# Performance work log

Hardware: AMD Instinct MI355X
Metric: run time of the kernel (lower is better)

The kernel has to match this reference:

```python
import jax, jax.numpy as jnp
import numpy as np
from jax import lax

KS = 5            # patch kernel size
STRIDE = 4        # patch stride / scale ratio
SHIFTS = (2, 2)   # roll shifts before patch extraction
SOFTMAX_SCALE = 10.0
MID_CH = 64
BAND_HS = 8


def same_pad(x, k, s):
    """TensorFlow-style SAME padding for kernel k, stride s (NCHW)."""
    H, W = x.shape[-2], x.shape[-1]
    oh, ow = -(-H // s), -(-W // s)
    ph = max(0, (oh - 1) * s + k - H)
    pw = max(0, (ow - 1) * s + k - W)
    return jnp.pad(x, ((0, 0), (0, 0), (ph // 2, ph - ph // 2), (pw // 2, pw - pw // 2)))


def extract_patches(x, k, s, shifts):
    """torch.nn.Unfold equivalent with SAME padding and roll -> [N, L, C, k, k]."""
    x = same_pad(x, k, s)
    x = jnp.roll(x, shifts[0], axis=2)
    x = jnp.roll(x, shifts[1], axis=3)
    p = lax.conv_general_dilated_patches(
        x, (k, k), (s, s), 'VALID', dimension_numbers=('NCHW', 'OIHW', 'NCHW'))
    N, _, Hn, Wn = p.shape
    C = x.shape[1]
    # channel ordering is (C, kh, kw) channel-slowest, matching torch unfold
    return p.reshape(N, C, k, k, Hn * Wn).transpose(0, 4, 1, 2, 3)


def conv3(x, w, b):
    """3x3 conv, padding=1, bias + LeakyReLU(0.01) (BasicBlock)."""
    y = lax.conv_general_dilated(x, w, (1, 1), [(1, 1), (1, 1)],
                                 dimension_numbers=('NCHW', 'OIHW', 'NCHW'))
    return jax.nn.leaky_relu(y + b[None, :, None, None], 0.01)


def setup_inputs() -> dict:
    key = jax.random.key(0)
    ks = jax.random.split(key, 11)
    f32 = jnp.float32
    return {
        'ms':   jax.random.normal(ks[0], (2, BAND_HS, 96, 96), f32),
        'pan':  jax.random.normal(ks[1], (2, 1, 384, 384), f32),
        'pan2': jax.random.normal(ks[2], (2, 1, 96, 96), f32),
        'wq': jax.random.normal(ks[3], (MID_CH, 1, 3, 3), f32) * 0.1,
        'bq': jax.random.normal(ks[4], (MID_CH,), f32) * 0.02,
        'wk': jax.random.normal(ks[5], (MID_CH, 1, 3, 3), f32) * 0.1,
        'bk': jax.random.normal(ks[6], (MID_CH,), f32) * 0.02,
        'wv': jax.random.normal(ks[7], (BAND_HS, BAND_HS, 3, 3), f32) * 0.1,
        'bv': jax.random.normal(ks[8], (BAND_HS,), f32) * 0.02,
        'wr': jax.random.normal(ks[9], (BAND_HS, BAND_HS, 3, 3), f32) * 0.1,
        'br': jax.random.normal(ks[10], (BAND_HS,), f32) * 0.02,
    }


def reference(ms, pan, pan2, wq, bq, wk, bk, wv, bv, wr, br):
    k_fea = conv3(pan2, wk, bk)                       # [N, mid, h, w]
    q_fea = conv3(pan, wq, bq)                        # [N, mid, H, W]
    v_fea = conv3(ms, wv, bv)                         # [N, band, h, w]

    k_patch = extract_patches(k_fea, KS, STRIDE, SHIFTS)  # [N, L, mid, ks, ks]
    v_patch = extract_patches(v_fea, KS, STRIDE, SHIFTS)  # [N, L, band, ks, ks]

    def attend(q, kp, vp):
        # q: [mid, H, W]; kp: [L, mid, ks, ks]; vp: [L, band, ks, ks]
        norms = jnp.sqrt(jnp.sum(kp * kp, axis=(1, 2, 3)))      # per-patch L2 norms
        k0 = kp / jnp.max(norms)                                # global-max normalization
        q0 = same_pad(q[None], KS, STRIDE)                      # [1, mid, Hp, Wp]
        scores = lax.conv_general_dilated(
            q0, k0, (STRIDE, STRIDE), 'VALID',
            dimension_numbers=('NCHW', 'OIHW', 'NCHW'))          # [1, L, H', W']
        attn = jax.nn.softmax(scores * SOFTMAX_SCALE, axis=1)
        # conv_transpose2d(attn, vp, stride) == dilated conv with flipped, transposed kernel
        wT = jnp.flip(vp, (2, 3)).transpose(1, 0, 2, 3)          # [band, L, ks, ks]
        out = lax.conv_general_dilated(
            attn, wT, (1, 1), [(KS - 1, KS - 1)] * 2,
            lhs_dilation=(STRIDE, STRIDE),
            dimension_numbers=('NCHW', 'OIHW', 'NCHW'))          # [1, band, Ho, Wo]
        return out[0] / 6.0

    res = jax.vmap(attend)(q_fea, k_patch, v_patch)   # [N, band, Ho, Wo]
    return conv3(res, wr, br)
```

## Files before the change

### kernel.cpp

```cpp
#include <hip/hip_runtime.h>
#include <math.h>


typedef _Float16 f16;
typedef _Float16 f16x8 __attribute__((ext_vector_type(8)));
typedef float f32x4 __attribute__((ext_vector_type(4)));

namespace csa {
constexpr int NB   = 2;
constexpr int MID  = 64;
constexpr int BAND = 8;
constexpr int HK   = 96;
constexpr int HQ   = 384;
constexpr int HQP  = 385;
constexpr int LN   = 24;
constexpr int L    = 576;
constexpr int LP   = 640;
constexpr int PS   = 96 * 96;
constexpr int KDIM = MID * 25;
constexpr int VDIM = BAND * 25;
constexpr int MV   = 256;
constexpr int HO   = 385;
constexpr size_t QCLN = (size_t)HQP * HQP * MID;

constexpr size_t align256(size_t x) { return (x + 255) & ~(size_t)255; }
constexpr size_t OFF_QCL  = 0;
constexpr size_t OFF_KCL  = align256(OFF_QCL + (size_t)NB*QCLN*2);
constexpr size_t OFF_VFEA = align256(OFF_KCL + (size_t)NB*HK*HK*MID*2);
constexpr size_t OFF_N2   = align256(OFF_VFEA + (size_t)NB*BAND*HK*HK*4);
constexpr size_t OFF_SC   = align256(OFF_N2   + (size_t)NB*L*4);
constexpr size_t OFF_KM   = align256(OFF_SC   + 256);
constexpr size_t OFF_VT   = align256(OFF_KM   + (size_t)NB*LP*KDIM*2);
constexpr size_t OFF_ST   = align256(OFF_VT   + (size_t)NB*MV*L*2);
constexpr size_t OFF_AT   = align256(OFF_ST   + (size_t)NB*PS*LP*4);
constexpr size_t OFF_D    = align256(OFF_AT   + (size_t)NB*PS*L*2);
constexpr size_t OFF_RES  = align256(OFF_D    + (size_t)NB*MV*PS*4);
}
using namespace csa;

__global__ __launch_bounds__(256) void csa_conv_cl(
    const float* __restrict__ in, const float* __restrict__ w,
    const float* __restrict__ b, f16* __restrict__ out, int H, int Hout) {
  int id = blockIdx.x * 256 + threadIdx.x;
  int total = NB * Hout * Hout;
  if (id >= total) return;
  int x = id % Hout;
  int t = id / Hout;
  int y = t % Hout;
  int n = t / Hout;
  f16* op = out + (size_t)id * MID;
  if (y >= H || x >= H) {
    f16x8 z = {0, 0, 0, 0, 0, 0, 0, 0};
#pragma unroll
    for (int c8 = 0; c8 < 8; ++c8) *(f16x8*)(op + c8 * 8) = z;
    return;
  }
  const float* ip = in + (size_t)n * H * H;
  float p[9];
#pragma unroll
  for (int dy = 0; dy < 3; ++dy)
#pragma unroll
    for (int dx = 0; dx < 3; ++dx) {
      int yy = y + dy - 1, xx = x + dx - 1;
      p[dy * 3 + dx] = (yy >= 0 && yy < H && xx >= 0 && xx < H)
                           ? ip[(size_t)yy * H + xx] : 0.f;
    }
#pragma unroll
  for (int c8 = 0; c8 < 8; ++c8) {
    f16x8 o;
#pragma unroll
    for (int e = 0; e < 8; ++e) {
      int co = c8 * 8 + e;
      float acc = b[co];
#pragma unroll
      for (int k = 0; k < 9; ++k) acc = fmaf(p[k], w[co * 9 + k], acc);
      o[e] = (f16)(acc > 0.f ? acc : 0.01f * acc);
    }
    *(f16x8*)(op + c8 * 8) = o;
  }
}

__global__ __launch_bounds__(256) void csa_conv3_8x8(
    const float* __restrict__ in, const float* __restrict__ w,
    const float* __restrict__ b, float* __restrict__ out, int H, int W) {
  int id = blockIdx.x * 256 + threadIdx.x;
  int total = NB * H * W;
  if (id >= total) return;
  int x = id % W;
  int t = id / W;
  int y = t % H;
  int n = t / H;
  const float* ip = in + (size_t)n * BAND * H * W;
  float p[BAND][9];
#pragma unroll
  for (int ci = 0; ci < BAND; ++ci)
#pragma unroll
    for (int dy = 0; dy < 3; ++dy)
#pragma unroll
      for (int dx = 0; dx < 3; ++dx) {
        int yy = y + dy - 1, xx = x + dx - 1;
        p[ci][dy * 3 + dx] = (yy >= 0 && yy < H && xx >= 0 && xx < W)
                                 ? ip[((size_t)ci * H + yy) * W + xx] : 0.f;
      }
  float* op = out + ((size_t)n * BAND * H + y) * W + x;
  for (int co = 0; co < BAND; ++co) {
    float acc = b[co];
#pragma unroll
    for (int ci = 0; ci < BAND; ++ci)
#pragma unroll
      for (int k = 0; k < 9; ++k)
        acc = fmaf(p[ci][k], w[(co * BAND + ci) * 9 + k], acc);
    acc = acc > 0.f ? acc : 0.01f * acc;
    op[(size_t)co * H * W] = acc;
  }
}

__global__ __launch_bounds__(256) void csa_build_patches(
    const f16* __restrict__ kcl, const float* __restrict__ v_fea,
    f16* __restrict__ Kmat, f16* __restrict__ Vt, float* __restrict__ n2) {
  int blk = blockIdx.x;
  int n = blk / LP;
  int l = blk % LP;
  int tid = threadIdx.x;
  f16* krow = Kmat + ((size_t)n * LP + l) * KDIM;
  if (l >= L) {
    f16x8 z = {0, 0, 0, 0, 0, 0, 0, 0};
    for (int ch = tid; ch < 200; ch += 256) *(f16x8*)(krow + ch * 8) = z;
    return;
  }
  int i = l / LN, j = l % LN;
  const f16* kn = kcl + (size_t)n * HK * HK * MID;
  float ss = 0.f;
  for (int ch = tid; ch < 200; ch += 256) {
    int khkw = ch >> 3;
    int c0 = (ch & 7) * 8;
    int kh = khkw / 5, kw = khkw % 5;
    int r = (4 * i + kh + 95) % 97;
    int cc = (4 * j + kw + 95) % 97;
    f16x8 v = {0, 0, 0, 0, 0, 0, 0, 0};
    if (r < HK && cc < HK)
      v = *(const f16x8*)(kn + ((size_t)r * HK + cc) * MID + c0);
#pragma unroll
    for (int e = 0; e < 8; ++e) {
      float f = (float)v[e];
      ss += f * f;
    }
    *(f16x8*)(krow + ch * 8) = v;
  }
  for (int m = tid; m < MV; m += 256) {
    float v = 0.f;
    if (m < VDIM) {
      int kw = m % 5;
      int t = m / 5;
      int kh = t % 5;
      int c = t / 5;
      int r = (4 * i + kh + 95) % 97;
      int cc = (4 * j + kw + 95) % 97;
      v = (r < HK && cc < HK)
              ? v_fea[(((size_t)n * BAND + c) * HK + r) * HK + cc] : 0.f;
    }
    Vt[((size_t)n * MV + m) * L + l] = (f16)v;
  }
  __shared__ float red[256];
  red[tid] = ss;
  __syncthreads();
  for (int s = 128; s > 0; s >>= 1) {
    if (tid < s) red[tid] += red[tid + s];
    __syncthreads();
  }
  if (tid == 0) n2[n * L + l] = red[0];
}

__global__ __launch_bounds__(256) void csa_max_scale(
    const float* __restrict__ n2, float* __restrict__ scale) {
  int n = blockIdx.x;
  int tid = threadIdx.x;
  float m = 0.f;
  for (int l = tid; l < L; l += 256) m = fmaxf(m, n2[n * L + l]);
  __shared__ float red[256];
  red[tid] = m;
  __syncthreads();
  for (int s = 128; s > 0; s >>= 1) {
    if (tid < s) red[tid] = fmaxf(red[tid], red[tid + s]);
    __syncthreads();
  }
  if (tid == 0) scale[n] = 10.f / sqrtf(red[0]);
}

__device__ __forceinline__ void gl_lds16(const f16* g, f16* s) {
  __builtin_amdgcn_global_load_lds(
      (const __attribute__((address_space(1))) void*)g,
      (__attribute__((address_space(3))) void*)s, 16, 0, 0);
}

__global__ __launch_bounds__(256) void csa_gemm1(
    const f16* __restrict__ qcl, const f16* __restrict__ Km,
    float* __restrict__ C) {
  __shared__ __attribute__((aligned(16))) f16 As[4096];
  __shared__ __attribute__((aligned(16))) f16 Bs[4096];
  const int tid = threadIdx.x;
  const int w = tid >> 6;
  const int l = tid & 63;
  const int q = l >> 4;
  const int r = l & 15;
  const int nb = blockIdx.z;
  qcl += (size_t)nb * QCLN;
  Km += (size_t)nb * LP * KDIM;
  C += (size_t)nb * (size_t)PS * LP;
  const int bm = blockIdx.y * 128;
  const int bn = blockIdx.x * 128;
  const int wm = (w >> 1) * 64;
  const int wn = (w & 1) * 64;

  f32x4 acc[4][4];
#pragma unroll
  for (int i = 0; i < 4; ++i)
#pragma unroll
    for (int j = 0; j < 4; ++j) {
      f32x4 z = {0.f, 0.f, 0.f, 0.f};
      acc[i][j] = z;
    }

  const int p0 = bm + w * 16 + r;
  const int y0 = p0 / 96, x0 = p0 % 96;
  const int p1 = p0 + 64;
  const int y1 = p1 / 96, x1 = p1 % 96;
  const f16* a0 = qcl + ((size_t)(4 * y0) * HQP + 4 * x0) * MID + q * 8;
  const f16* a1 = qcl + ((size_t)(4 * y1) * HQP + 4 * x1) * MID + q * 8;
  const f16* gb0 = Km + (size_t)(bn + w * 16 + r) * KDIM + q * 8;
  const f16* gb1 = gb0 + (size_t)64 * KDIM;
  f16* lA0 = As + w * 512;
  f16* lA1 = As + 2048 + w * 512;
  f16* lB0 = Bs + w * 512;
  f16* lB1 = Bs + 2048 + w * 512;
  const int am = (w >> 1) * 4;
  const int bnn = (w & 1) * 4;

  int t = 0;
  for (int kh = 0; kh < 5; ++kh) {
    for (int kw = 0; kw < 5; ++kw) {
      const size_t offA = ((size_t)kh * HQP + kw) * MID;
#pragma unroll
      for (int half = 0; half < 2; ++half, ++t) {
        const size_t oA = offA + half * 32;
        const size_t oB = (size_t)t * 32;
        gl_lds16(a0 + oA, lA0);
        gl_lds16(a1 + oA, lA1);
        gl_lds16(gb0 + oB, lB0);
        gl_lds16(gb1 + oB, lB1);
        __syncthreads();
        f16x8 af[4], bf[4];
#pragma unroll
        for (int u = 0; u < 4; ++u) {
          af[u] = *(const f16x8*)&As[(am + u) * 512 + q * 128 + r * 8];
          bf[u] = *(const f16x8*)&Bs[(bnn + u) * 512 + q * 128 + r * 8];
        }
#pragma unroll
        for (int i = 0; i < 4; ++i)
#pragma unroll
          for (int j = 0; j < 4; ++j)
            acc[i][j] = __builtin_amdgcn_mfma_f32_16x16x32_f16(af[i], bf[j],
                                                               acc[i][j], 0, 0, 0);
        __syncthreads();
      }
    }
  }
  const int cn = bn + wn + r;
#pragma unroll
  for (int i = 0; i < 4; ++i) {
    int rm = bm + wm + i * 16 + q * 4;
#pragma unroll
    for (int j = 0; j < 4; ++j)
#pragma unroll
      for (int rr = 0; rr < 4; ++rr)
        C[(size_t)(rm + rr) * LP + cn + j * 16] = acc[i][j][rr];
  }
}

__global__ __launch_bounds__(256) void csa_gemm_f16(
    const f16* __restrict__ A, const f16* __restrict__ Bt,
    float* __restrict__ C, int M, int N, int K,
    size_t strideA, size_t strideB, size_t strideC) {
  __shared__ __attribute__((aligned(16))) f16 As[4096];
  __shared__ __attribute__((aligned(16))) f16 Bs[4096];
  const int tid = threadIdx.x;
  const int w = tid >> 6;
  const int l = tid & 63;
  const int q = l >> 4;
  const int r = l & 15;
  const int nb = blockIdx.z;
  A += (size_t)nb * strideA;
  Bt += (size_t)nb * strideB;
  C += (size_t)nb * strideC;
  const int bm = blockIdx.y * 128;
  const int bn = blockIdx.x * 128;
  const int wm = (w >> 1) * 64;
  const int wn = (w & 1) * 64;

  f32x4 acc[4][4];
#pragma unroll
  for (int i = 0; i < 4; ++i)
#pragma unroll
    for (int j = 0; j < 4; ++j) {
      f32x4 z = {0.f, 0.f, 0.f, 0.f};
      acc[i][j] = z;
    }

  const f16* ga0 = A + (size_t)(bm + w * 16 + r) * K + q * 8;
  const f16* ga1 = ga0 + (size_t)64 * K;
  const f16* gb0 = Bt + (size_t)(bn + w * 16 + r) * K + q * 8;
  const f16* gb1 = gb0 + (size_t)64 * K;
  f16* lA0 = As + w * 512;
  f16* lA1 = As + 2048 + w * 512;
  f16* lB0 = Bs + w * 512;
  f16* lB1 = Bs + 2048 + w * 512;
  const int am = (w >> 1) * 4;
  const int bnn = (w & 1) * 4;

  for (int k0 = 0; k0 < K; k0 += 32) {
    gl_lds16(ga0 + k0, lA0);
    gl_lds16(ga1 + k0, lA1);
    gl_lds16(gb0 + k0, lB0);
    gl_lds16(gb1 + k0, lB1);
    __syncthreads();
    f16x8 af[4], bf[4];
#pragma unroll
    for (int u = 0; u < 4; ++u) {
      af[u] = *(const f16x8*)&As[(am + u) * 512 + q * 128 + r * 8];
      bf[u] = *(const f16x8*)&Bs[(bnn + u) * 512 + q * 128 + r * 8];
    }
#pragma unroll
    for (int i = 0; i < 4; ++i)
#pragma unroll
      for (int j = 0; j < 4; ++j)
        acc[i][j] =
            __builtin_amdgcn_mfma_f32_16x16x32_f16(af[i], bf[j], acc[i][j], 0, 0, 0);
    __syncthreads();
  }

  const int cn = bn + wn + r;
#pragma unroll
  for (int i = 0; i < 4; ++i) {
    int rm = bm + wm + i * 16 + q * 4;
#pragma unroll
    for (int j = 0; j < 4; ++j)
#pragma unroll
      for (int rr = 0; rr < 4; ++rr)
        C[(size_t)(rm + rr) * N + cn + j * 16] = acc[i][j][rr];
  }
}

__global__ __launch_bounds__(256) void csa_softmax(
    const float* __restrict__ scoresT, const float* __restrict__ scale,
    f16* __restrict__ attnT) {
  const int wv = threadIdx.x >> 6;
  const int lane = threadIdx.x & 63;
  const int p = blockIdx.x * 4 + wv;
  const int n = blockIdx.y;
  const float sc = scale[n];
  const float* row = scoresT + ((size_t)n * PS + p) * LP;
  float v[9];
  float m = -1e30f;
#pragma unroll
  for (int j = 0; j < 9; ++j) {
    v[j] = row[lane + j * 64] * sc;
    m = fmaxf(m, v[j]);
  }
#pragma unroll
  for (int off = 32; off > 0; off >>= 1) m = fmaxf(m, __shfl_xor(m, off));
  float e[9], s = 0.f;
#pragma unroll
  for (int j = 0; j < 9; ++j) {
    e[j] = __expf(v[j] - m);
    s += e[j];
  }
#pragma unroll
  for (int off = 32; off > 0; off >>= 1) s += __shfl_xor(s, off);
  const float inv = 1.f / s;
  f16* orow = attnT + ((size_t)n * PS + p) * L;
#pragma unroll
  for (int j = 0; j < 9; ++j) orow[lane + j * 64] = (f16)(e[j] * inv);
}

__global__ __launch_bounds__(256) void csa_gather(
    const float* __restrict__ D, float* __restrict__ res) {
  int id = blockIdx.x * 256 + threadIdx.x;
  if (id >= NB * BAND * HO * HO) return;
  int ox = id % HO;
  int t = id / HO;
  int oy = t % HO;
  t = t / HO;
  int co = t % BAND;
  int n = t / BAND;
  const float* Dn = D + (size_t)n * MV * PS;
  float s = 0.f;
  int kh0 = oy & 3;
  int kw0 = ox & 3;
  for (int kh = kh0; kh < 5; kh += 4) {
    int y = (oy - kh) >> 2;
    if (y < 0 || y >= 96) continue;
    for (int kw = kw0; kw < 5; kw += 4) {
      int x = (ox - kw) >> 2;
      if (x < 0 || x >= 96) continue;
      s += Dn[(size_t)(co * 25 + kh * 5 + kw) * PS + y * 96 + x];
    }
  }
  res[id] = s * (1.f / 6.f);
}

extern "C" void kernel_launch(void* const* d_in, const int* in_sizes, int n_in,
                              void* d_out, int out_size, void* d_ws,
                              size_t ws_size, hipStream_t stream) {
  const float* ms   = (const float*)d_in[0];
  const float* pan  = (const float*)d_in[1];
  const float* pan2 = (const float*)d_in[2];
  const float* wq = (const float*)d_in[3];
  const float* bq = (const float*)d_in[4];
  const float* wk = (const float*)d_in[5];
  const float* bk = (const float*)d_in[6];
  const float* wv = (const float*)d_in[7];
  const float* bv = (const float*)d_in[8];
  const float* wr = (const float*)d_in[9];
  const float* br = (const float*)d_in[10];
  float* out = (float*)d_out;

  char* ws = (char*)d_ws;
  f16*   qcl   = (f16*)(ws + OFF_QCL);
  f16*   kcl   = (f16*)(ws + OFF_KCL);
  float* v_fea = (float*)(ws + OFF_VFEA);
  float* n2    = (float*)(ws + OFF_N2);
  float* scale = (float*)(ws + OFF_SC);
  f16*   Kmat  = (f16*)(ws + OFF_KM);
  f16*   Vt    = (f16*)(ws + OFF_VT);
  float* scoT  = (float*)(ws + OFF_ST);
  f16*   attnT = (f16*)(ws + OFF_AT);
  float* Dm    = (float*)(ws + OFF_D);
  float* res   = (float*)(ws + OFF_RES);

  dim3 b256(256);
  csa_conv_cl<<<dim3((NB * HQP * HQP + 255) / 256), b256, 0, stream>>>(
      pan, wq, bq, qcl, HQ, HQP);
  csa_conv_cl<<<dim3((NB * HK * HK + 255) / 256), b256, 0, stream>>>(
      pan2, wk, bk, kcl, HK, HK);
  csa_conv3_8x8<<<dim3((NB * HK * HK + 255) / 256), b256, 0, stream>>>(
      ms, wv, bv, v_fea, HK, HK);
  csa_build_patches<<<dim3(NB * LP), b256, 0, stream>>>(kcl, v_fea, Kmat, Vt,
                                                        n2);
  csa_max_scale<<<dim3(NB), b256, 0, stream>>>(n2, scale);

  csa_gemm1<<<dim3(LP / 128, PS / 128, NB), b256, 0, stream>>>(qcl, Kmat,
                                                               scoT);

  csa_softmax<<<dim3(PS / 4, NB), b256, 0, stream>>>(scoT, scale, attnT);

  csa_gemm_f16<<<dim3(PS / 128, MV / 128, NB), b256, 0, stream>>>(
      Vt, attnT, Dm, MV, PS, L,
      (size_t)MV * L, (size_t)PS * L, (size_t)MV * PS);

  csa_gather<<<dim3((NB * BAND * HO * HO + 255) / 256), b256, 0, stream>>>(
      Dm, res);
  csa_conv3_8x8<<<dim3((NB * HO * HO + 255) / 256), b256, 0, stream>>>(
      res, wr, br, out, HO, HO);
}
```

Before: 302.6 us.

## Store Q features in stride-4 phase-split layout for contiguous GEMM A loads

The query conv output is now written in a polyphase layout [n][x-phase][y][x/4][ch], so the stride-4 patch rows read by the scores GEMM sit next to each other in memory. Before, each lane read 128-byte channel vectors spaced 4 pixels apart. The wider, coalesced A-tile loads are meant to cut wasted memory traffic in gemm1. In exchange the conv writes a slightly larger buffer with an extra padded column, the address math becomes more complex, and the zero padding at the edges has to be handled correctly.

```diff
diff --git a/kernel.cpp b/kernel.cpp
--- a/kernel.cpp
+++ b/kernel.cpp
@@ -13,6 +13,7 @@
 constexpr int HK   = 96;
 constexpr int HQ   = 384;
 constexpr int HQP  = 385;
+constexpr int XI   = 97;
 constexpr int LN   = 24;
 constexpr int L    = 576;
 constexpr int LP   = 640;
@@ -21,11 +22,11 @@
 constexpr int VDIM = BAND * 25;
 constexpr int MV   = 256;
 constexpr int HO   = 385;
-constexpr size_t QCLN = (size_t)HQP * HQP * MID;
+constexpr size_t QPSN = (size_t)4 * HQP * XI * MID;
 
 constexpr size_t align256(size_t x) { return (x + 255) & ~(size_t)255; }
-constexpr size_t OFF_QCL  = 0;
-constexpr size_t OFF_KCL  = align256(OFF_QCL + (size_t)NB*QCLN*2);
+constexpr size_t OFF_QPS  = 0;
+constexpr size_t OFF_KCL  = align256(OFF_QPS + (size_t)NB*QPSN*2);
 constexpr size_t OFF_VFEA = align256(OFF_KCL + (size_t)NB*HK*HK*MID*2);
 constexpr size_t OFF_N2   = align256(OFF_VFEA + (size_t)NB*BAND*HK*HK*4);
 constexpr size_t OFF_SC   = align256(OFF_N2   + (size_t)NB*L*4);
@@ -38,23 +39,62 @@
 }
 using namespace csa;
 
+__global__ __launch_bounds__(256) void csa_convq_ps(
+    const float* __restrict__ in, const float* __restrict__ w,
+    const float* __restrict__ b, f16* __restrict__ out) {
+  int id = blockIdx.x * 256 + threadIdx.x;
+  int total = NB * 4 * HQP * XI;
+  if (id >= total) return;
+  int xi = id % XI;
+  int t = id / XI;
+  int yp = t % HQP;
+  t /= HQP;
+  int f = t % 4;
+  int n = t / 4;
+  int xp = 4 * xi + f;
+  f16* op = out + (size_t)id * MID;
+  if (yp >= HQ || xp >= HQ) {
+    f16x8 z = {0, 0, 0, 0, 0, 0, 0, 0};
+#pragma unroll
+    for (int c8 = 0; c8 < 8; ++c8) *(f16x8*)(op + c8 * 8) = z;
+    return;
+  }
+  const float* ip = in + (size_t)n * HQ * HQ;
+  float p[9];
+#pragma unroll
+  for (int dy = 0; dy < 3; ++dy)
+#pragma unroll
+    for (int dx = 0; dx < 3; ++dx) {
+      int yy = yp + dy - 1, xx = xp + dx - 1;
+      p[dy * 3 + dx] = (yy >= 0 && yy < HQ && xx >= 0 && xx < HQ)
+                           ? ip[(size_t)yy * HQ + xx] : 0.f;
+    }
+#pragma unroll
+  for (int c8 = 0; c8 < 8; ++c8) {
+    f16x8 o;
+#pragma unroll
+    for (int e = 0; e < 8; ++e) {
+      int co = c8 * 8 + e;
+      float acc = b[co];
+#pragma unroll
+      for (int k = 0; k < 9; ++k) acc = fmaf(p[k], w[co * 9 + k], acc);
+      o[e] = (f16)(acc > 0.f ? acc : 0.01f * acc);
+    }
+    *(f16x8*)(op + c8 * 8) = o;
+  }
+}
+
 __global__ __launch_bounds__(256) void csa_conv_cl(
     const float* __restrict__ in, const float* __restrict__ w,
-    const float* __restrict__ b, f16* __restrict__ out, int H, int Hout) {
+    const float* __restrict__ b, f16* __restrict__ out, int H) {
   int id = blockIdx.x * 256 + threadIdx.x;
-  int total = NB * Hout * Hout;
+  int total = NB * H * H;
   if (id >= total) return;
-  int x = id % Hout;
-  int t = id / Hout;
-  int y = t % Hout;
-  int n = t / Hout;
+  int x = id % H;
+  int t = id / H;
+  int y = t % H;
+  int n = t / H;
   f16* op = out + (size_t)id * MID;
-  if (y >= H || x >= H) {
-    f16x8 z = {0, 0, 0, 0, 0, 0, 0, 0};
-#pragma unroll
-    for (int c8 = 0; c8 < 8; ++c8) *(f16x8*)(op + c8 * 8) = z;
-    return;
-  }
   const float* ip = in + (size_t)n * H * H;
   float p[9];
 #pragma unroll
@@ -142,8 +182,8 @@
       v = *(const f16x8*)(kn + ((size_t)r * HK + cc) * MID + c0);
 #pragma unroll
     for (int e = 0; e < 8; ++e) {
-      float f = (float)v[e];
-      ss += f * f;
+      float fv = (float)v[e];
+      ss += fv * fv;
     }
     *(f16x8*)(krow + ch * 8) = v;
   }
@@ -194,7 +234,7 @@
 }
 
 __global__ __launch_bounds__(256) void csa_gemm1(
-    const f16* __restrict__ qcl, const f16* __restrict__ Km,
+    const f16* __restrict__ qps, const f16* __restrict__ Km,
     float* __restrict__ C) {
   __shared__ __attribute__((aligned(16))) f16 As[4096];
   __shared__ __attribute__((aligned(16))) f16 Bs[4096];
@@ -204,7 +244,7 @@
   const int q = l >> 4;
   const int r = l & 15;
   const int nb = blockIdx.z;
-  qcl += (size_t)nb * QCLN;
+  qps += (size_t)nb * QPSN;
   Km += (size_t)nb * LP * KDIM;
   C += (size_t)nb * (size_t)PS * LP;
   const int bm = blockIdx.y * 128;
@@ -221,12 +261,12 @@
       acc[i][j] = z;
     }
 
-  const int p0 = bm + w * 16 + r;
-  const int y0 = p0 / 96, x0 = p0 % 96;
-  const int p1 = p0 + 64;
-  const int y1 = p1 / 96, x1 = p1 % 96;
-  const f16* a0 = qcl + ((size_t)(4 * y0) * HQP + 4 * x0) * MID + q * 8;
-  const f16* a1 = qcl + ((size_t)(4 * y1) * HQP + 4 * x1) * MID + q * 8;
+  const int pg0 = bm + w * 16;
+  const int y0 = pg0 / 96, x0 = pg0 % 96;
+  const int pg1 = pg0 + 64;
+  const int y1 = pg1 / 96, x1 = pg1 % 96;
+  const int la = r * MID + q * 8;
+
   const f16* gb0 = Km + (size_t)(bn + w * 16 + r) * KDIM + q * 8;
   const f16* gb1 = gb0 + (size_t)64 * KDIM;
   f16* lA0 = As + w * 512;
@@ -239,13 +279,16 @@
   int t = 0;
   for (int kh = 0; kh < 5; ++kh) {
     for (int kw = 0; kw < 5; ++kw) {
-      const size_t offA = ((size_t)kh * HQP + kw) * MID;
+      const size_t u0 =
+          (((size_t)(kw & 3) * HQP + (4 * y0 + kh)) * XI + x0 + (kw >> 2)) * MID;
+      const size_t u1 =
+          (((size_t)(kw & 3) * HQP + (4 * y1 + kh)) * XI + x1 + (kw >> 2)) * MID;
 #pragma unroll
       for (int half = 0; half < 2; ++half, ++t) {
-        const size_t oA = offA + half * 32;
+        const size_t oA = (size_t)half * 32 + la;
         const size_t oB = (size_t)t * 32;
-        gl_lds16(a0 + oA, lA0);
-        gl_lds16(a1 + oA, lA1);
+        gl_lds16(qps + u0 + oA, lA0);
+        gl_lds16(qps + u1 + oA, lA1);
         gl_lds16(gb0 + oB, lB0);
         gl_lds16(gb1 + oB, lB1);
         __syncthreads();
@@ -425,7 +468,7 @@
   float* out = (float*)d_out;
 
   char* ws = (char*)d_ws;
-  f16*   qcl   = (f16*)(ws + OFF_QCL);
+  f16*   qps   = (f16*)(ws + OFF_QPS);
   f16*   kcl   = (f16*)(ws + OFF_KCL);
   float* v_fea = (float*)(ws + OFF_VFEA);
   float* n2    = (float*)(ws + OFF_N2);
@@ -438,17 +481,17 @@
   float* res   = (float*)(ws + OFF_RES);
 
   dim3 b256(256);
-  csa_conv_cl<<<dim3((NB * HQP * HQP + 255) / 256), b256, 0, stream>>>(
-      pan, wq, bq, qcl, HQ, HQP);
+  csa_convq_ps<<<dim3((NB * 4 * HQP * XI + 255) / 256), b256, 0, stream>>>(
+      pan, wq, bq, qps);
   csa_conv_cl<<<dim3((NB * HK * HK + 255) / 256), b256, 0, stream>>>(
-      pan2, wk, bk, kcl, HK, HK);
+      pan2, wk, bk, kcl, HK);
   csa_conv3_8x8<<<dim3((NB * HK * HK + 255) / 256), b256, 0, stream>>>(
       ms, wv, bv, v_fea, HK, HK);
   csa_build_patches<<<dim3(NB * LP), b256, 0, stream>>>(kcl, v_fea, Kmat, Vt,
                                                         n2);
   csa_max_scale<<<dim3(NB), b256, 0, stream>>>(n2, scale);
 
-  csa_gemm1<<<dim3(LP / 128, PS / 128, NB), b256, 0, stream>>>(qcl, Kmat,
+  csa_gemm1<<<dim3(LP / 128, PS / 128, NB), b256, 0, stream>>>(qps, Kmat,
                                                                scoT);
 
   csa_softmax<<<dim3(PS / 4, NB), b256, 0, stream>>>(scoT, scale, attnT);
```

Measured after the change: 279.4 us. -7.7%, faster.
